# Performance work log

Measured on AMD Instinct MI355X. Metric: run time of the kernel, lower is better.

The kernel has to match this reference:

```python
import jax, jax.numpy as jnp
import numpy as np

B, H, T, D = 2, 16, 2048, 64


def setup_inputs() -> dict:
    key = jax.random.key(0)
    kq, kk, kv, km = jax.random.split(key, 4)
    q = jax.random.normal(kq, (B, H, T, D), dtype=jnp.float32)
    k = jax.random.normal(kk, (B, H, T, D), dtype=jnp.float32)
    v = jax.random.normal(kv, (B, H, T, D), dtype=jnp.float32)
    mask = jax.random.randint(km, (T, T), 0, 2, dtype=jnp.int32)
    return {"q": q, "k": k, "v": v, "mask": mask}


def reference(q, k, v, mask):
    d_k = q.shape[-1]
    scale = jnp.asarray(d_k, q.dtype) ** -0.5
    # (B,H,T,D) @ (B,H,D,T) -> (B,H,T,T)
    scores = jnp.einsum("bhtd,bhsd->bhts", q * scale, k)
    # mask broadcast over (B,H); masked positions set to -1e9 as in torch code
    scores = jnp.where(mask[None, None, :, :] == 0, jnp.asarray(-1e9, scores.dtype), scores)
    attn = jax.nn.softmax(scores, axis=-1)
    # (B,H,T,T) @ (B,H,T,D) -> (B,H,T,D)
    out = jnp.einsum("bhts,bhsd->bhtd", attn, v)
    return (out, attn)
```

## Files before the change

### kernel.cpp

```cpp
#include <hip/hip_runtime.h>
#include <hip/hip_bf16.h>
#include <cstddef>

#define T_SEQ 2048
#define D_HEAD 64
#define BC 64
#define NKT (T_SEQ / BC)
#define PAD 72

typedef __bf16 bf16x8 __attribute__((ext_vector_type(8)));
typedef float f32x4 __attribute__((ext_vector_type(4)));
typedef unsigned short u16x8 __attribute__((ext_vector_type(8)));

__device__ __forceinline__ unsigned short f2bf(float f) {
  __bf16 h = (__bf16)f;
  return __builtin_bit_cast(unsigned short, h);
}
__device__ __forceinline__ bf16x8 ldfrag(const unsigned short* p) {
  u16x8 t = *(const u16x8*)p;
  return __builtin_bit_cast(bf16x8, t);
}
__device__ __forceinline__ f32x4 mfma16(bf16x8 a, bf16x8 b, f32x4 c) {
  return __builtin_amdgcn_mfma_f32_16x16x32_bf16(a, b, c, 0, 0, 0);
}
__device__ __forceinline__ void bar_sync() {
  asm volatile("" ::: "memory");
  __builtin_amdgcn_s_barrier();
  asm volatile("" ::: "memory");
}
__device__ __forceinline__ void lds_fence() {
  asm volatile("s_waitcnt lgkmcnt(0)" ::: "memory");
}
__device__ __forceinline__ float exp2_hw(float x) { return __builtin_amdgcn_exp2f(x); }
__device__ __forceinline__ float log2_hw(float x) { return __builtin_amdgcn_logf(x); }

__global__ __launch_bounds__(256) void mask_pack(const int* __restrict__ maskg,
                                                 unsigned* __restrict__ mp) {
  const size_t total = (size_t)T_SEQ * T_SEQ;
  size_t idx = (size_t)blockIdx.x * blockDim.x + threadIdx.x;
  const size_t stride = (size_t)gridDim.x * blockDim.x;
  const int lane = threadIdx.x & 63;
  for (; idx < total; idx += stride) {
    int mv = maskg[idx];
    unsigned long long b = __ballot(mv != 0);
    if (lane == 0)       mp[idx >> 5] = (unsigned)b;
    else if (lane == 32) mp[idx >> 5] = (unsigned)(b >> 32);
  }
}

__global__ __launch_bounds__(256, 5) void attn_fused2(
    const float* __restrict__ qg, const float* __restrict__ kg,
    const float* __restrict__ vg, const unsigned* __restrict__ mpk,
    float* __restrict__ outg, float* __restrict__ attng)
{
  __shared__ unsigned short ks[BC][PAD];
  __shared__ unsigned short vt[D_HEAD][PAD];
  __shared__ unsigned short ps[64][PAD];

  const int bid = blockIdx.x;
  const int lin = (bid & 7) * 128 + (bid >> 3);
  const int bh  = lin >> 5;
  const int strip = lin & 31;

  const int tid  = threadIdx.x;
  const int lane = tid & 63;
  const int wid  = tid >> 6;
  const int lr = lane & 15, lh = lane >> 4;
  const int r0 = strip * 64 + wid * 16;
  const int sv = tid >> 2;
  const int sc4 = (tid & 3) << 4;
  const int vt7 = tid & 7;
  const int vs2 = (tid >> 3) * 2;

  const float C = 0.18033688011112042f;
  const float* qb = qg + (size_t)bh * T_SEQ * D_HEAD;
  const float* kb = kg + (size_t)bh * T_SEQ * D_HEAD;
  const float* vb = vg + (size_t)bh * T_SEQ * D_HEAD;
  const int ROWW = T_SEQ / 32;
  const f32x4 zero4 = {0.f, 0.f, 0.f, 0.f};

  bf16x8 qf[2];
  {
    const float* qr = qb + (size_t)(r0 + lr) * D_HEAD;
    #pragma unroll
    for (int kk = 0; kk < 2; ++kk) {
      float4 a = *(const float4*)(qr + kk * 32 + lh * 8);
      float4 b = *(const float4*)(qr + kk * 32 + lh * 8 + 4);
      u16x8 u;
      u[0] = f2bf(a.x); u[1] = f2bf(a.y); u[2] = f2bf(a.z); u[3] = f2bf(a.w);
      u[4] = f2bf(b.x); u[5] = f2bf(b.y); u[6] = f2bf(b.z); u[7] = f2bf(b.w);
      qf[kk] = __builtin_bit_cast(bf16x8, u);
    }
  }

  f32x4 acc[4];
  #pragma unroll
  for (int nt = 0; nt < 4; ++nt) acc[nt] = zero4;
  float psum_s = 0.f;

  for (int kt = 0; kt < NKT; ++kt) {
    const int n0 = kt * BC;
    bar_sync();
    {
      const float* ksrc = kb + (size_t)(n0 + sv) * D_HEAD + sc4;
      float4 k0 = *(const float4*)(ksrc + 0),  k1 = *(const float4*)(ksrc + 4);
      float4 k2 = *(const float4*)(ksrc + 8),  k3 = *(const float4*)(ksrc + 12);
      u16x8 w0, w1;
      w0[0]=f2bf(k0.x); w0[1]=f2bf(k0.y); w0[2]=f2bf(k0.z); w0[3]=f2bf(k0.w);
      w0[4]=f2bf(k1.x); w0[5]=f2bf(k1.y); w0[6]=f2bf(k1.z); w0[7]=f2bf(k1.w);
      w1[0]=f2bf(k2.x); w1[1]=f2bf(k2.y); w1[2]=f2bf(k2.z); w1[3]=f2bf(k2.w);
      w1[4]=f2bf(k3.x); w1[5]=f2bf(k3.y); w1[6]=f2bf(k3.z); w1[7]=f2bf(k3.w);
      *(u16x8*)&ks[sv][sc4 + 0] = w0;
      *(u16x8*)&ks[sv][sc4 + 8] = w1;
    }
    {
      const float* v0 = vb + (size_t)(n0 + vs2) * D_HEAD + vt7;
      const float* v1 = v0 + D_HEAD;
      #pragma unroll
      for (int j = 0; j < 8; ++j) {
        const float a = v0[8 * j];
        const float b = v1[8 * j];
        const unsigned w = (unsigned)f2bf(a) | ((unsigned)f2bf(b) << 16);
        *(unsigned*)&vt[vt7 + 8 * j][vs2] = w;
      }
    }
    const unsigned mw0 = mpk[(size_t)(r0 + lr) * ROWW + kt * 2];
    const unsigned mw1 = mpk[(size_t)(r0 + lr) * ROWW + kt * 2 + 1];
    lds_fence(); bar_sync();

    f32x4 st[4];
    #pragma unroll
    for (int nt = 0; nt < 4; ++nt) st[nt] = zero4;
    #pragma unroll
    for (int kk = 0; kk < 2; ++kk) {
      bf16x8 kf[4];
      #pragma unroll
      for (int nt = 0; nt < 4; ++nt) kf[nt] = ldfrag(&ks[nt * 16 + lr][kk * 32 + lh * 8]);
      #pragma unroll
      for (int nt = 0; nt < 4; ++nt) st[nt] = mfma16(kf[nt], qf[kk], st[nt]);
    }
    #pragma unroll
    for (int nt = 0; nt < 4; ++nt) {
      const unsigned w = (nt & 2) ? mw1 : mw0;
      float p[4];
      #pragma unroll
      for (int r = 0; r < 4; ++r) {
        const int bit = (nt & 1) * 16 + 4 * lh + r;
        p[r] = ((w >> bit) & 1) ? exp2_hw(st[nt][r] * C) : 0.f;
        psum_s += p[r];
      }
      uint2 u;
      u.x = (unsigned)f2bf(p[0]) | ((unsigned)f2bf(p[1]) << 16);
      u.y = (unsigned)f2bf(p[2]) | ((unsigned)f2bf(p[3]) << 16);
      *(uint2*)&ps[wid * 16 + lr][nt * 16 + 4 * lh] = u;
    }
    lds_fence();
    #pragma unroll
    for (int kk = 0; kk < 2; ++kk) {
      const bf16x8 pa = ldfrag(&ps[wid * 16 + lr][kk * 32 + lh * 8]);
      #pragma unroll
      for (int nt = 0; nt < 4; ++nt) {
        const bf16x8 vf = ldfrag(&vt[nt * 16 + lr][kk * 32 + lh * 8]);
        acc[nt] = mfma16(pa, vf, acc[nt]);
      }
    }
  }

  psum_s += __shfl_xor(psum_s, 16);
  psum_s += __shfl_xor(psum_s, 32);
  const float iv_s = 1.0f / psum_s;
  float ivq[4], lg2ivq[4];
  #pragma unroll
  for (int r = 0; r < 4; ++r) {
    ivq[r] = __shfl(iv_s, 4 * lh + r);
    lg2ivq[r] = log2_hw(ivq[r]);
  }

  float* ob = outg + (size_t)(bh * T_SEQ + r0) * D_HEAD;
  #pragma unroll
  for (int nt = 0; nt < 4; ++nt)
    #pragma unroll
    for (int r = 0; r < 4; ++r)
      ob[(size_t)(4 * lh + r) * D_HEAD + nt * 16 + lr] = acc[nt][r] * ivq[r];

  float* ab = attng + (size_t)(bh * T_SEQ + r0) * T_SEQ;
  for (int kt = 0; kt < NKT; ++kt) {
    const int n0 = kt * BC;
    bar_sync();
    {
      const float* ksrc = kb + (size_t)(n0 + sv) * D_HEAD + sc4;
      float4 k0 = *(const float4*)(ksrc + 0),  k1 = *(const float4*)(ksrc + 4);
      float4 k2 = *(const float4*)(ksrc + 8),  k3 = *(const float4*)(ksrc + 12);
      u16x8 w0, w1;
      w0[0]=f2bf(k0.x); w0[1]=f2bf(k0.y); w0[2]=f2bf(k0.z); w0[3]=f2bf(k0.w);
      w0[4]=f2bf(k1.x); w0[5]=f2bf(k1.y); w0[6]=f2bf(k1.z); w0[7]=f2bf(k1.w);
      w1[0]=f2bf(k2.x); w1[1]=f2bf(k2.y); w1[2]=f2bf(k2.z); w1[3]=f2bf(k2.w);
      w1[4]=f2bf(k3.x); w1[5]=f2bf(k3.y); w1[6]=f2bf(k3.z); w1[7]=f2bf(k3.w);
      *(u16x8*)&ks[sv][sc4 + 0] = w0;
      *(u16x8*)&ks[sv][sc4 + 8] = w1;
    }
    unsigned mw[4][2];
    #pragma unroll
    for (int r = 0; r < 4; ++r) {
      const size_t mrow = (size_t)(r0 + 4 * lh + r) * ROWW + kt * 2;
      mw[r][0] = mpk[mrow];
      mw[r][1] = mpk[mrow + 1];
    }
    lds_fence(); bar_sync();

    f32x4 sc_[4];
    #pragma unroll
    for (int nt = 0; nt < 4; ++nt) sc_[nt] = zero4;
    #pragma unroll
    for (int kk = 0; kk < 2; ++kk) {
      bf16x8 kf[4];
      #pragma unroll
      for (int nt = 0; nt < 4; ++nt) kf[nt] = ldfrag(&ks[nt * 16 + lr][kk * 32 + lh * 8]);
      #pragma unroll
      for (int nt = 0; nt < 4; ++nt) sc_[nt] = mfma16(qf[kk], kf[nt], sc_[nt]);
    }
    #pragma unroll
    for (int r = 0; r < 4; ++r) {
      float* arow = ab + (size_t)(4 * lh + r) * T_SEQ + n0;
      #pragma unroll
      for (int nt = 0; nt < 4; ++nt) {
        const int mv = (mw[r][nt >> 1] >> ((nt & 1) * 16 + lr)) & 1;
        const float p = mv ? exp2_hw(__builtin_fmaf(sc_[nt][r], C, lg2ivq[r])) : 0.f;
        __builtin_nontemporal_store(p, arow + nt * 16 + lr);
      }
    }
  }
}

__global__ __launch_bounds__(512, 2) void attn_fused_fb(
    const float* __restrict__ qg, const float* __restrict__ kg,
    const float* __restrict__ vg, const int* __restrict__ maskg,
    float* __restrict__ outg, float* __restrict__ attng)
{
  __shared__ unsigned short qs[128][PAD];
  __shared__ unsigned short ks[64][PAD];
  __shared__ unsigned short vt[64][PAD];
  __shared__ unsigned short pp[128][PAD];
  __shared__ float rsum[128];
  int bid = blockIdx.x;
  int lin = (bid & 7) * 64 + (bid >> 3);
  int bh = lin >> 4, br0 = (lin & 15) * 128;
  const int tid = threadIdx.x, lane = tid & 63, wid = tid >> 6;
  const int wm = wid >> 1, wn = wid & 1, lr = lane & 15, lh = lane >> 4;
  const float scale = 0.125f;
  const float* qb = qg + ((size_t)bh * T_SEQ + br0) * D_HEAD;
  const float* kbp = kg + (size_t)bh * T_SEQ * D_HEAD;
  const float* vbp = vg + (size_t)bh * T_SEQ * D_HEAD;
  if (tid < 128) rsum[tid] = 0.f;
  #pragma unroll
  for (int it = 0; it < 4; ++it) {
    int idx = it * 512 + tid;
    int r = idx >> 4, c = (idx & 15) << 2;
    float4 f = *(const float4*)(qb + (size_t)r * D_HEAD + c);
    *(ushort4*)&qs[r][c] = make_ushort4(f2bf(f.x), f2bf(f.y), f2bf(f.z), f2bf(f.w));
  }
  f32x4 acc_o[2][2];
  const f32x4 zero4 = {0.f, 0.f, 0.f, 0.f};
  #pragma unroll
  for (int a = 0; a < 2; ++a)
    #pragma unroll
    for (int b = 0; b < 2; ++b) acc_o[a][b] = zero4;
  float psum[2][4] = {{0.f,0.f,0.f,0.f},{0.f,0.f,0.f,0.f}};
  __syncthreads();
  for (int kt = 0; kt < NKT; ++kt) {
    const int kb0 = kt * 64;
    #pragma unroll
    for (int it = 0; it < 2; ++it) {
      int idx = it * 512 + tid;
      int r = idx >> 4, c = (idx & 15) << 2;
      float4 f = *(const float4*)(kbp + (size_t)(kb0 + r) * D_HEAD + c);
      *(ushort4*)&ks[r][c] = make_ushort4(f2bf(f.x), f2bf(f.y), f2bf(f.z), f2bf(f.w));
      float4 g = *(const float4*)(vbp + (size_t)(kb0 + r) * D_HEAD + c);
      vt[c+0][r] = f2bf(g.x); vt[c+1][r] = f2bf(g.y);
      vt[c+2][r] = f2bf(g.z); vt[c+3][r] = f2bf(g.w);
    }
    __syncthreads();
    f32x4 sc[2][2];
    #pragma unroll
    for (int a = 0; a < 2; ++a)
      #pragma unroll
      for (int b = 0; b < 2; ++b) sc[a][b] = zero4;
    #pragma unroll
    for (int kk = 0; kk < 2; ++kk) {
      const int ke = kk * 32 + lh * 8;
      bf16x8 af[2], bfq[2];
      #pragma unroll
      for (int mt = 0; mt < 2; ++mt) af[mt] = ldfrag(&qs[wm*32 + mt*16 + lr][ke]);
      #pragma unroll
      for (int nt = 0; nt < 2; ++nt) bfq[nt] = ldfrag(&ks[wn*32 + nt*16 + lr][ke]);
      #pragma unroll
      for (int mt = 0; mt < 2; ++mt)
        #pragma unroll
        for (int nt = 0; nt < 2; ++nt)
          sc[mt][nt] = mfma16(af[mt], bfq[nt], sc[mt][nt]);
    }
    #pragma unroll
    for (int mt = 0; mt < 2; ++mt)
      #pragma unroll
      for (int nt = 0; nt < 2; ++nt)
        #pragma unroll
        for (int r = 0; r < 4; ++r) {
          int row = wm*32 + mt*16 + lh*4 + r, col = wn*32 + nt*16 + lr;
          int mv = maskg[(size_t)(br0 + row) * T_SEQ + (kb0 + col)];
          float p = mv ? __expf(sc[mt][nt][r] * scale) : 0.f;
          psum[mt][r] += p;
          pp[row][col] = f2bf(p);
        }
    __syncthreads();
    #pragma unroll
    for (int kk = 0; kk < 2; ++kk) {
      const int ke = kk * 32 + lh * 8;
      bf16x8 pa[2], vf[2];
      #pragma unroll
      for (int mt = 0; mt < 2; ++mt) pa[mt] = ldfrag(&pp[wm*32 + mt*16 + lr][ke]);
      #pragma unroll
      for (int nt = 0; nt < 2; ++nt) vf[nt] = ldfrag(&vt[wn*32 + nt*16 + lr][ke]);
      #pragma unroll
      for (int mt = 0; mt < 2; ++mt)
        #pragma unroll
        for (int nt = 0; nt < 2; ++nt)
          acc_o[mt][nt] = mfma16(pa[mt], vf[nt], acc_o[mt][nt]);
    }
    __syncthreads();
  }
  #pragma unroll
  for (int mt = 0; mt < 2; ++mt)
    #pragma unroll
    for (int r = 0; r < 4; ++r) {
      float sv = psum[mt][r];
      sv += __shfl_xor(sv, 1); sv += __shfl_xor(sv, 2);
      sv += __shfl_xor(sv, 4); sv += __shfl_xor(sv, 8);
      if (lr == 0) atomicAdd(&rsum[wm*32 + mt*16 + lh*4 + r], sv);
    }
  __syncthreads();
  float invs[2][4];
  #pragma unroll
  for (int mt = 0; mt < 2; ++mt)
    #pragma unroll
    for (int r = 0; r < 4; ++r)
      invs[mt][r] = 1.0f / rsum[wm*32 + mt*16 + lh*4 + r];
  float* ob = outg + ((size_t)bh * T_SEQ + br0) * D_HEAD;
  #pragma unroll
  for (int mt = 0; mt < 2; ++mt)
    #pragma unroll
    for (int nt = 0; nt < 2; ++nt)
      #pragma unroll
      for (int r = 0; r < 4; ++r) {
        int row = wm*32 + mt*16 + lh*4 + r, col = wn*32 + nt*16 + lr;
        ob[(size_t)row * D_HEAD + col] = acc_o[mt][nt][r] * invs[mt][r];
      }
  float* ab = attng + (size_t)bh * T_SEQ * T_SEQ + (size_t)br0 * T_SEQ;
  for (int kt = 0; kt < NKT; ++kt) {
    const int kb0 = kt * 64;
    __syncthreads();
    #pragma unroll
    for (int it = 0; it < 2; ++it) {
      int idx = it * 512 + tid;
      int r = idx >> 4, c = (idx & 15) << 2;
      float4 f = *(const float4*)(kbp + (size_t)(kb0 + r) * D_HEAD + c);
      *(ushort4*)&ks[r][c] = make_ushort4(f2bf(f.x), f2bf(f.y), f2bf(f.z), f2bf(f.w));
    }
    __syncthreads();
    f32x4 sc[2][2];
    #pragma unroll
    for (int a = 0; a < 2; ++a)
      #pragma unroll
      for (int b = 0; b < 2; ++b) sc[a][b] = zero4;
    #pragma unroll
    for (int kk = 0; kk < 2; ++kk) {
      const int ke = kk * 32 + lh * 8;
      bf16x8 af[2], bfq[2];
      #pragma unroll
      for (int mt = 0; mt < 2; ++mt) af[mt] = ldfrag(&qs[wm*32 + mt*16 + lr][ke]);
      #pragma unroll
      for (int nt = 0; nt < 2; ++nt) bfq[nt] = ldfrag(&ks[wn*32 + nt*16 + lr][ke]);
      #pragma unroll
      for (int mt = 0; mt < 2; ++mt)
        #pragma unroll
        for (int nt = 0; nt < 2; ++nt)
          sc[mt][nt] = mfma16(af[mt], bfq[nt], sc[mt][nt]);
    }
    #pragma unroll
    for (int mt = 0; mt < 2; ++mt)
      #pragma unroll
      for (int nt = 0; nt < 2; ++nt)
        #pragma unroll
        for (int r = 0; r < 4; ++r) {
          int row = wm*32 + mt*16 + lh*4 + r, col = wn*32 + nt*16 + lr;
          int mv = maskg[(size_t)(br0 + row) * T_SEQ + (kb0 + col)];
          float p = mv ? __expf(sc[mt][nt][r] * scale) * invs[mt][r] : 0.f;
          ab[(size_t)row * T_SEQ + kb0 + col] = p;
        }
  }
}

extern "C" void kernel_launch(void* const* d_in, const int* in_sizes, int n_in,
                              void* d_out, int out_size, void* d_ws, size_t ws_size,
                              hipStream_t stream) {
  const float* q = (const float*)d_in[0];
  const float* k = (const float*)d_in[1];
  const float* v = (const float*)d_in[2];
  const int* mask = (const int*)d_in[3];
  float* out = (float*)d_out;
  float* attn = out + (size_t)2 * 16 * T_SEQ * D_HEAD;

  const size_t mpk_bytes = (size_t)T_SEQ * T_SEQ / 8;
  if (ws_size >= mpk_bytes) {
    unsigned* mp = (unsigned*)d_ws;
    mask_pack<<<dim3(2048), 256, 0, stream>>>(mask, mp);
    attn_fused2<<<dim3(1024), 256, 0, stream>>>(q, k, v, mp, out, attn);
  } else {
    attn_fused_fb<<<dim3(512), 512, 0, stream>>>(q, k, v, mask, out, attn);
  }
}
```

Baseline: 189.4 us.

## Move PV accumulation into second pass, making first pass row-sum only

```diff
diff --git a/kernel.cpp b/kernel.cpp
--- a/kernel.cpp
+++ b/kernel.cpp
@@ -48,7 +48,7 @@
   }
 }
 
-__global__ __launch_bounds__(256, 5) void attn_fused2(
+__global__ __launch_bounds__(256, 4) void attn_fused6(
     const float* __restrict__ qg, const float* __restrict__ kg,
     const float* __restrict__ vg, const unsigned* __restrict__ mpk,
     float* __restrict__ outg, float* __restrict__ attng)
@@ -93,9 +93,6 @@
     }
   }
 
-  f32x4 acc[4];
-  #pragma unroll
-  for (int nt = 0; nt < 4; ++nt) acc[nt] = zero4;
   float psum_s = 0.f;
 
   for (int kt = 0; kt < NKT; ++kt) {
@@ -113,17 +110,6 @@
       *(u16x8*)&ks[sv][sc4 + 0] = w0;
       *(u16x8*)&ks[sv][sc4 + 8] = w1;
     }
-    {
-      const float* v0 = vb + (size_t)(n0 + vs2) * D_HEAD + vt7;
-      const float* v1 = v0 + D_HEAD;
-      #pragma unroll
-      for (int j = 0; j < 8; ++j) {
-        const float a = v0[8 * j];
-        const float b = v1[8 * j];
-        const unsigned w = (unsigned)f2bf(a) | ((unsigned)f2bf(b) << 16);
-        *(unsigned*)&vt[vt7 + 8 * j][vs2] = w;
-      }
-    }
     const unsigned mw0 = mpk[(size_t)(r0 + lr) * ROWW + kt * 2];
     const unsigned mw1 = mpk[(size_t)(r0 + lr) * ROWW + kt * 2 + 1];
     lds_fence(); bar_sync();
@@ -142,26 +128,10 @@
     #pragma unroll
     for (int nt = 0; nt < 4; ++nt) {
       const unsigned w = (nt & 2) ? mw1 : mw0;
-      float p[4];
       #pragma unroll
       for (int r = 0; r < 4; ++r) {
         const int bit = (nt & 1) * 16 + 4 * lh + r;
-        p[r] = ((w >> bit) & 1) ? exp2_hw(st[nt][r] * C) : 0.f;
-        psum_s += p[r];
-      }
-      uint2 u;
-      u.x = (unsigned)f2bf(p[0]) | ((unsigned)f2bf(p[1]) << 16);
-      u.y = (unsigned)f2bf(p[2]) | ((unsigned)f2bf(p[3]) << 16);
-      *(uint2*)&ps[wid * 16 + lr][nt * 16 + 4 * lh] = u;
-    }
-    lds_fence();
-    #pragma unroll
-    for (int kk = 0; kk < 2; ++kk) {
-      const bf16x8 pa = ldfrag(&ps[wid * 16 + lr][kk * 32 + lh * 8]);
-      #pragma unroll
-      for (int nt = 0; nt < 4; ++nt) {
-        const bf16x8 vf = ldfrag(&vt[nt * 16 + lr][kk * 32 + lh * 8]);
-        acc[nt] = mfma16(pa, vf, acc[nt]);
+        psum_s += ((w >> bit) & 1) ? exp2_hw(st[nt][r] * C) : 0.f;
       }
     }
   }
@@ -176,12 +146,9 @@
     lg2ivq[r] = log2_hw(ivq[r]);
   }
 
-  float* ob = outg + (size_t)(bh * T_SEQ + r0) * D_HEAD;
-  #pragma unroll
-  for (int nt = 0; nt < 4; ++nt)
-    #pragma unroll
-    for (int r = 0; r < 4; ++r)
-      ob[(size_t)(4 * lh + r) * D_HEAD + nt * 16 + lr] = acc[nt][r] * ivq[r];
+  f32x4 acc[4];
+  #pragma unroll
+  for (int nt = 0; nt < 4; ++nt) acc[nt] = zero4;
 
   float* ab = attng + (size_t)(bh * T_SEQ + r0) * T_SEQ;
   for (int kt = 0; kt < NKT; ++kt) {
@@ -198,38 +165,81 @@
       w1[4]=f2bf(k3.x); w1[5]=f2bf(k3.y); w1[6]=f2bf(k3.z); w1[7]=f2bf(k3.w);
       *(u16x8*)&ks[sv][sc4 + 0] = w0;
       *(u16x8*)&ks[sv][sc4 + 8] = w1;
-    }
-    unsigned mw[4][2];
+      const float* v0 = vb + (size_t)(n0 + vs2) * D_HEAD + vt7;
+      const float* v1 = v0 + D_HEAD;
+      #pragma unroll
+      for (int j = 0; j < 8; ++j) {
+        const unsigned w = (unsigned)f2bf(v0[8 * j]) | ((unsigned)f2bf(v1[8 * j]) << 16);
+        *(unsigned*)&vt[vt7 + 8 * j][vs2] = w;
+      }
+    }
+    const unsigned mw0 = mpk[(size_t)(r0 + lr) * ROWW + kt * 2];
+    const unsigned mw1 = mpk[(size_t)(r0 + lr) * ROWW + kt * 2 + 1];
+    unsigned md[4][2];
     #pragma unroll
     for (int r = 0; r < 4; ++r) {
       const size_t mrow = (size_t)(r0 + 4 * lh + r) * ROWW + kt * 2;
-      mw[r][0] = mpk[mrow];
-      mw[r][1] = mpk[mrow + 1];
+      md[r][0] = mpk[mrow];
+      md[r][1] = mpk[mrow + 1];
     }
     lds_fence(); bar_sync();
 
-    f32x4 sc_[4];
-    #pragma unroll
-    for (int nt = 0; nt < 4; ++nt) sc_[nt] = zero4;
+    f32x4 st[4], sd[4];
+    #pragma unroll
+    for (int nt = 0; nt < 4; ++nt) { st[nt] = zero4; sd[nt] = zero4; }
     #pragma unroll
     for (int kk = 0; kk < 2; ++kk) {
       bf16x8 kf[4];
       #pragma unroll
       for (int nt = 0; nt < 4; ++nt) kf[nt] = ldfrag(&ks[nt * 16 + lr][kk * 32 + lh * 8]);
       #pragma unroll
-      for (int nt = 0; nt < 4; ++nt) sc_[nt] = mfma16(qf[kk], kf[nt], sc_[nt]);
+      for (int nt = 0; nt < 4; ++nt) {
+        st[nt] = mfma16(kf[nt], qf[kk], st[nt]);
+        sd[nt] = mfma16(qf[kk], kf[nt], sd[nt]);
+      }
+    }
+    #pragma unroll
+    for (int nt = 0; nt < 4; ++nt) {
+      const unsigned w = (nt & 2) ? mw1 : mw0;
+      float p[4];
+      #pragma unroll
+      for (int r = 0; r < 4; ++r) {
+        const int bit = (nt & 1) * 16 + 4 * lh + r;
+        p[r] = ((w >> bit) & 1) ? exp2_hw(st[nt][r] * C) : 0.f;
+      }
+      uint2 u;
+      u.x = (unsigned)f2bf(p[0]) | ((unsigned)f2bf(p[1]) << 16);
+      u.y = (unsigned)f2bf(p[2]) | ((unsigned)f2bf(p[3]) << 16);
+      *(uint2*)&ps[wid * 16 + lr][nt * 16 + 4 * lh] = u;
+    }
+    lds_fence();
+    #pragma unroll
+    for (int kk = 0; kk < 2; ++kk) {
+      const bf16x8 pa = ldfrag(&ps[wid * 16 + lr][kk * 32 + lh * 8]);
+      #pragma unroll
+      for (int nt = 0; nt < 4; ++nt) {
+        const bf16x8 vf = ldfrag(&vt[nt * 16 + lr][kk * 32 + lh * 8]);
+        acc[nt] = mfma16(pa, vf, acc[nt]);
+      }
     }
     #pragma unroll
     for (int r = 0; r < 4; ++r) {
       float* arow = ab + (size_t)(4 * lh + r) * T_SEQ + n0;
       #pragma unroll
       for (int nt = 0; nt < 4; ++nt) {
-        const int mv = (mw[r][nt >> 1] >> ((nt & 1) * 16 + lr)) & 1;
-        const float p = mv ? exp2_hw(__builtin_fmaf(sc_[nt][r], C, lg2ivq[r])) : 0.f;
+        const int mv = (md[r][nt >> 1] >> ((nt & 1) * 16 + lr)) & 1;
+        const float p = mv ? exp2_hw(__builtin_fmaf(sd[nt][r], C, lg2ivq[r])) : 0.f;
         __builtin_nontemporal_store(p, arow + nt * 16 + lr);
       }
     }
   }
+
+  float* ob = outg + (size_t)(bh * T_SEQ + r0) * D_HEAD;
+  #pragma unroll
+  for (int nt = 0; nt < 4; ++nt)
+    #pragma unroll
+    for (int r = 0; r < 4; ++r)
+      ob[(size_t)(4 * lh + r) * D_HEAD + nt * 16 + lr] = acc[nt][r] * ivq[r];
 }
 
 __global__ __launch_bounds__(512, 2) void attn_fused_fb(
@@ -413,7 +423,7 @@
   if (ws_size >= mpk_bytes) {
     unsigned* mp = (unsigned*)d_ws;
     mask_pack<<<dim3(2048), 256, 0, stream>>>(mask, mp);
-    attn_fused2<<<dim3(1024), 256, 0, stream>>>(q, k, v, mp, out, attn);
+    attn_fused6<<<dim3(1024), 256, 0, stream>>>(q, k, v, mp, out, attn);
   } else {
     attn_fused_fb<<<dim3(512), 512, 0, stream>>>(q, k, v, mask, out, attn);
   }
```

Result: slower. 204.4 us (+7.9%).
